# Kernel optimization log

Measured on AMD Instinct MI355X. Metric: run time of the kernel, lower is better.

## Reference

```python
import jax, jax.numpy as jnp
import numpy as np

R_EPS = 1e-15

def _sdf_net(x, W1, b1, W2, b2):
    h = jax.nn.relu(x @ W1 + b1)
    return h @ W2 + b2  # [..., 1+feat]

def _fd_gradient(x, W1, b1, W2, b2, eps):
    # central finite differences of the SDF along the 3 axes
    offs = eps * jnp.eye(3, dtype=x.dtype)              # [3,3]
    xp = x[None, :, :] + offs[:, None, :]               # [3,P,3]
    xm = x[None, :, :] - offs[:, None, :]
    sp = _sdf_net(xp, W1, b1, W2, b2)[..., 0]           # [3,P]
    sm = _sdf_net(xm, W1, b1, W2, b2)[..., 0]
    return ((sp - sm) / (2.0 * eps)).T                  # [P,3]

def _softplus100(x):
    # torch.nn.Softplus(beta=100)
    return jax.nn.softplus(100.0 * x) / 100.0

def _exclusive_cumprod(a):
    ones = jnp.ones_like(a[:, :1])
    return jnp.cumprod(jnp.concatenate([ones, a], -1), -1)[:, :-1]

def _sample_pdf(bins, weights, n_samples):
    # bins [R,K], weights [R,K-1]; deterministic inverse-CDF sampling (det=True)
    weights = weights + 1e-5
    pdf = weights / jnp.sum(weights, -1, keepdims=True)
    cdf = jnp.cumsum(pdf, -1)
    cdf = jnp.concatenate([jnp.zeros_like(cdf[:, :1]), cdf], -1)  # [R,K]
    K = cdf.shape[-1]
    u = jnp.linspace(0.5 / n_samples, 1.0 - 0.5 / n_samples, n_samples, dtype=bins.dtype)
    u = jnp.broadcast_to(u[None], (bins.shape[0], n_samples))
    inds = jax.vmap(lambda c, uu: jnp.searchsorted(c, uu, side='right'))(cdf, u)
    below = jnp.clip(inds - 1, 0, K - 1)
    above = jnp.clip(inds, 0, K - 1)
    cdf_b = jnp.take_along_axis(cdf, below, -1)
    cdf_a = jnp.take_along_axis(cdf, above, -1)
    bin_b = jnp.take_along_axis(bins, below, -1)
    bin_a = jnp.take_along_axis(bins, above, -1)
    denom = cdf_a - cdf_b
    denom = jnp.where(denom < 1e-5, jnp.ones_like(denom), denom)
    t = (u - cdf_b) / denom
    return bin_b + t * (bin_a - bin_b)

def _forward(rays_o, rays_d, W1, b1, W2, b2, Wc1, bc1, Wc2, bc2, inv_s_param,
             num_steps, upsample_steps, bound):
    B, N = rays_o.shape[:2]
    ro = rays_o.reshape(-1, 3)
    rd = rays_d.reshape(-1, 3)
    R = ro.shape[0]
    bnd = float(bound)
    # near/far from cube bound
    tmin = (-bnd - ro) / (rd + R_EPS)
    tmax = (bnd - ro) / (rd + R_EPS)
    near = jnp.max(jnp.minimum(tmin, tmax), -1, keepdims=True)
    far = jnp.min(jnp.maximum(tmin, tmax), -1, keepdims=True)
    near = jnp.maximum(near, 0.05)
    z = jnp.linspace(0.0, 1.0, num_steps, dtype=ro.dtype)[None]
    z_vals = near + (far - near) * z                     # [R,S0]
    sample_dist = (far - near) / num_steps               # [R,1]
    pts = ro[:, None, :] + rd[:, None, :] * z_vals[..., None]
    pts = jnp.clip(pts, -bnd, bnd)
    # --- coarse SDF pass + inverse-CDF importance resampling (torch.no_grad) ---
    sdf_c = _sdf_net(pts.reshape(-1, 3), W1, b1, W2, b2)[:, 0].reshape(R, num_steps)
    sdf_c = jax.lax.stop_gradient(sdf_c)
    d_c = z_vals[:, 1:] - z_vals[:, :-1]
    mid_sdf = 0.5 * (sdf_c[:, 1:] + sdf_c[:, :-1])
    cos_val = jnp.clip((sdf_c[:, 1:] - sdf_c[:, :-1]) / (d_c + 1e-5), -1e3, 0.0)
    prev_c = jax.nn.sigmoid((mid_sdf - cos_val * d_c * 0.5) * 64.0)
    next_c = jax.nn.sigmoid((mid_sdf + cos_val * d_c * 0.5) * 64.0)
    alpha_c = jnp.clip((prev_c - next_c + 1e-5) / (prev_c + 1e-5), 0.0, 1.0)
    w_c = alpha_c * _exclusive_cumprod(1.0 - alpha_c + 1e-7)
    new_z = jax.lax.stop_gradient(_sample_pdf(z_vals, w_c, upsample_steps))
    z_vals = jnp.sort(jnp.concatenate([z_vals, new_z], -1), -1)
    S = num_steps + upsample_steps
    # --- fine pass: deltas / midpoints / shading / NeuS compositing ---
    deltas = z_vals[:, 1:] - z_vals[:, :-1]
    deltas = jnp.concatenate([deltas, jnp.broadcast_to(sample_dist, (R, 1))], -1)
    z_mid = jnp.concatenate([z_vals[:, :-1] + 0.5 * deltas[:, :-1], z_vals[:, -1:]], -1)
    new_pts = ro[:, None, :] + rd[:, None, :] * z_mid[..., None]
    new_pts = jnp.clip(new_pts, -bnd, bnd)
    flat_pts = new_pts.reshape(-1, 3)                    # [R*S,3]
    out = _sdf_net(flat_pts, W1, b1, W2, b2)
    sdf = out[:, :1]
    feat = out[:, 1:]
    grad = _fd_gradient(flat_pts, W1, b1, W2, b2, 0.005)  # eps=0.005*(1-ratio), ratio=0
    normal = grad / (1e-5 + jnp.linalg.norm(grad, axis=-1, keepdims=True))
    dirs = jnp.broadcast_to(rd[:, None, :], new_pts.shape).reshape(-1, 3)
    cin = jnp.concatenate([flat_pts, dirs, normal, feat], -1)
    color = jax.nn.sigmoid(jax.nn.relu(cin @ Wc1 + bc1) @ Wc2 + bc2)   # [R*S,3]
    inv_s = jnp.exp(10.0 * inv_s_param)                   # forward_variance()
    true_cos = jnp.sum(dirs * normal, -1, keepdims=True)
    iter_cos = -_softplus100(-true_cos)                   # cos_anneal_ratio = 1.0
    d_flat = deltas.reshape(-1, 1)
    prev_cdf = jax.nn.sigmoid((sdf - iter_cos * d_flat * 0.5) * inv_s)
    next_cdf = jax.nn.sigmoid((sdf + iter_cos * d_flat * 0.5) * inv_s)
    alpha = jnp.clip((prev_cdf - next_cdf + 1e-5) / (prev_cdf + 1e-5), 0.0, 1.0).reshape(R, S)
    weights = alpha * _exclusive_cumprod(1.0 - alpha + 1e-7)
    weights_sum = jnp.sum(weights, -1, keepdims=True)
    image = jnp.sum(color.reshape(R, S, 3) * weights[..., None], 1)
    image = image + (1.0 - weights_sum) * 1.0             # bg_color = 1
    return image.reshape(B, N, 3)

def setup_inputs() -> dict:
    key = jax.random.key(0)
    ks = jax.random.split(key, 8)
    B, N, H, F = 1, 4096, 64, 64
    rays_o = (jax.random.uniform(ks[0], (B, N, 3), jnp.float32) - 0.5) * 0.5
    d = jax.random.normal(ks[1], (B, N, 3), jnp.float32)
    rays_d = d / (1e-8 + jnp.linalg.norm(d, axis=-1, keepdims=True))
    def lin(k, i, o):
        return jax.random.normal(k, (i, o), jnp.float32) / np.sqrt(i).astype(np.float32)
    W1 = lin(ks[2], 3, H); b1 = jnp.zeros((H,), jnp.float32)
    W2 = lin(ks[3], H, 1 + F); b2 = jnp.zeros((1 + F,), jnp.float32)
    Wc1 = lin(ks[4], 9 + F, H); bc1 = jnp.zeros((H,), jnp.float32)
    Wc2 = lin(ks[5], H, 3); bc2 = jnp.zeros((3,), jnp.float32)
    inv_s_param = jnp.full((1,), 0.3, jnp.float32)
    return {"rays_o": rays_o, "rays_d": rays_d, "W1": W1, "b1": b1, "W2": W2, "b2": b2,
            "Wc1": Wc1, "bc1": bc1, "Wc2": Wc2, "bc2": bc2, "inv_s_param": inv_s_param,
            "num_steps": 64, "upsample_steps": 64, "bound": 1}

def reference(rays_o, rays_d, W1, b1, W2, b2, Wc1, bc1, Wc2, bc2, inv_s_param,
              num_steps, upsample_steps, bound):
    return _forward(rays_o, rays_d, W1, b1, W2, b2, Wc1, bc1, Wc2, bc2, inv_s_param,
                    num_steps, upsample_steps, bound)
```

## Files before the change

### kernel.cpp

```cpp
#include <hip/hip_runtime.h>
#include <hip/hip_bf16.h>
#include <cmath>

#define RAYS_PER_BLOCK 2
#define KS 84

#define OFF_W1    0
#define OFF_W1E   256
#define OFF_WC2   512
#define OFF_BC2   768
#define OFF_AF    772

typedef __attribute__((ext_vector_type(4))) short  short4v;
typedef __attribute__((ext_vector_type(8))) short  short8v;
typedef __attribute__((ext_vector_type(16))) float f32x16;

__device__ __forceinline__ float sigm(float x){ return 1.0f/(1.0f + expf(-x)); }
__device__ __forceinline__ float clampf(float x, float lo, float hi){ return fminf(fmaxf(x, lo), hi); }
__device__ __forceinline__ unsigned short f2bf(float x){
  __hip_bfloat16 h = __float2bfloat16(x);
  return *reinterpret_cast<unsigned short*>(&h);
}
__device__ __forceinline__ unsigned pk2(float a, float b){
  return (unsigned)f2bf(a) | ((unsigned)f2bf(b) << 16);
}
__device__ __forceinline__ short8v lds_load8(const unsigned short* p){
  short4v lo = *(const short4v*)p;
  short4v hi = *(const short4v*)(p + 4);
  short8v r;
  r[0]=lo[0]; r[1]=lo[1]; r[2]=lo[2]; r[3]=lo[3];
  r[4]=hi[0]; r[5]=hi[1]; r[6]=hi[2]; r[7]=hi[3];
  return r;
}

__global__ void prep_weights(const float* __restrict__ W1, const float* __restrict__ b1,
                             const float* __restrict__ W2, const float* __restrict__ b2,
                             const float* __restrict__ Wc1, const float* __restrict__ bc1,
                             const float* __restrict__ Wc2, const float* __restrict__ bc2,
                             float* __restrict__ ws)
{
  int g = blockIdx.x * blockDim.x + threadIdx.x;
  if (g < 640){
    int f = g >> 6, ln = g & 63;
    int mb = f / 5, kk = f - 5*mb;
    int c  = 32*mb + (ln & 31);
    int kbase = 16*kk + 8*(ln >> 5);
    unsigned short* dst = ((unsigned short*)(ws + OFF_AF)) + (size_t)g * 8;
    for (int j = 0; j < 8; ++j){
      int k = kbase + j;
      float v;
      if (k < 64){
        v = 0.f;
        for (int t = 0; t < 64; ++t) v += W2[k*65 + 1 + t] * Wc1[(9+t)*64 + c];
      } else if (k < 73){
        v = Wc1[(k-64)*64 + c];
      } else if (k == 73){
        v = bc1[c];
        for (int t = 0; t < 64; ++t) v += b2[1+t] * Wc1[(9+t)*64 + c];
      } else v = 0.f;
      dst[j] = f2bf(v);
    }
  } else if (g < 704){
    int j = g - 640;
    ws[OFF_W1 + 4*j + 0] = W1[j];
    ws[OFF_W1 + 4*j + 1] = W1[64+j];
    ws[OFF_W1 + 4*j + 2] = W1[128+j];
    ws[OFF_W1 + 4*j + 3] = b1[j];
  } else if (g < 768){
    int j = g - 704;
    ws[OFF_W1E + 4*j + 0] = 0.005f * W1[j];
    ws[OFF_W1E + 4*j + 1] = 0.005f * W1[64+j];
    ws[OFF_W1E + 4*j + 2] = 0.005f * W1[128+j];
    ws[OFF_W1E + 4*j + 3] = W2[j*65];
  } else if (g < 832){
    int j = g - 768;
    ws[OFF_WC2 + 4*j + 0] = Wc2[j*3+0];
    ws[OFF_WC2 + 4*j + 1] = Wc2[j*3+1];
    ws[OFF_WC2 + 4*j + 2] = Wc2[j*3+2];
    ws[OFF_WC2 + 4*j + 3] = 0.f;
  } else if (g < 836){
    int j = g - 832;
    ws[OFF_BC2 + j] = (j < 3) ? bc2[j] : b2[0];
  }
}

__global__ __launch_bounds__(256)
void neus_render(const float* __restrict__ rays_o, const float* __restrict__ rays_d,
                 const float* __restrict__ inv_s_p, const float* __restrict__ ws,
                 float* __restrict__ out)
{
  __shared__ unsigned short s_aext[4][64*KS];
  __shared__ float4 s_wc2[64];
  __shared__ float  s_z[RAYS_PER_BLOCK][64];
  __shared__ float  s_cdf[RAYS_PER_BLOCK][64];
  __shared__ float  s_newz[RAYS_PER_BLOCK][64];
  __shared__ float  s_zall[RAYS_PER_BLOCK][128];
  __shared__ float  s_red[RAYS_PER_BLOCK][2][4];
  __shared__ float  s_wtot[RAYS_PER_BLOCK][2];

  const int tid  = threadIdx.x;
  const int rs   = tid >> 7;
  const int lt   = tid & 127;
  const int lane = tid & 63;
  const int wir  = (tid >> 6) & 1;
  const int wv   = tid >> 6;
  const int ray  = blockIdx.x * RAYS_PER_BLOCK + rs;

  const float4* __restrict__ pW1  = (const float4*)(ws + OFF_W1);
  const float4* __restrict__ pW1E = (const float4*)(ws + OFF_W1E);
  const float*  __restrict__ pbc2 = ws + OFF_BC2;
  const float b20 = pbc2[3];

  if (tid < 64) s_wc2[tid] = ((const float4*)(ws + OFF_WC2))[tid];

  float ox = rays_o[ray*3], oy = rays_o[ray*3+1], oz = rays_o[ray*3+2];
  float dx = rays_d[ray*3], dy = rays_d[ray*3+1], dz = rays_d[ray*3+2];
  float tnx = (-1.f-ox)/(dx+1e-15f), tfx = (1.f-ox)/(dx+1e-15f);
  float tny = (-1.f-oy)/(dy+1e-15f), tfy = (1.f-oy)/(dy+1e-15f);
  float tnz = (-1.f-oz)/(dz+1e-15f), tfz = (1.f-oz)/(dz+1e-15f);
  float nearv = fmaxf(fmaxf(fminf(tnx,tfx), fminf(tny,tfy)), fminf(tnz,tfz));
  float farv  = fminf(fminf(fmaxf(tnx,tfx), fmaxf(tny,tfy)), fmaxf(tnz,tfz));
  nearv = fmaxf(nearv, 0.05f);
  const float sd = (farv - nearv) * (1.f/64.f);

  if (wir == 0){
    float zt = nearv + (farv-nearv) * ((float)lane * (1.f/63.f));
    float px = clampf(ox + dx*zt, -1.f, 1.f);
    float py = clampf(oy + dy*zt, -1.f, 1.f);
    float pz = clampf(oz + dz*zt, -1.f, 1.f);
    float acc = b20;
    #pragma unroll 8
    for (int j = 0; j < 64; ++j){
      float4 w = pW1[j];
      acc += fmaxf(px*w.x + py*w.y + pz*w.z + w.w, 0.f) * ws[OFF_W1E + 4*j + 3];
    }
    s_z[rs][lane] = zt;
    float s1  = __shfl_down(acc, 1);
    float zt1 = nearv + (farv-nearv) * ((float)(lane+1) * (1.f/63.f));
    float a_c = 0.f, qv = 1.f;
    if (lane < 63){
      float dc   = zt1 - zt;
      float mid  = 0.5f*(acc + s1);
      float cosv = clampf((s1-acc)/(dc+1e-5f), -1000.f, 0.f);
      float est  = cosv*dc*0.5f;
      float pcv  = sigm((mid-est)*64.f);
      float ncv  = sigm((mid+est)*64.f);
      a_c = clampf((pcv-ncv+1e-5f)/(pcv+1e-5f), 0.f, 1.f);
      qv  = 1.f - a_c + 1e-7f;
    }
    float p = qv;
    #pragma unroll
    for (int off = 1; off < 64; off <<= 1){
      float t = __shfl_up(p, off);
      if (lane >= off) p *= t;
    }
    float ec = __shfl_up(p, 1);
    if (lane == 0) ec = 1.f;
    float wvv = (lane < 63) ? (a_c*ec + 1e-5f) : 0.f;
    float tot = wvv;
    #pragma unroll
    for (int off = 32; off > 0; off >>= 1) tot += __shfl_xor(tot, off);
    float cs = wvv;
    #pragma unroll
    for (int off = 1; off < 64; off <<= 1){
      float t = __shfl_up(cs, off);
      if (lane >= off) cs += t;
    }
    if (lane == 0)  s_cdf[rs][0] = 0.f;
    if (lane < 63)  s_cdf[rs][lane+1] = cs / tot;
  }
  __syncthreads();

  if (wir == 0){
    float u = ((float)lane + 0.5f) * (1.f/64.f);
    int lo = 0, hi = 64;
    while (lo < hi){
      int m = (lo+hi) >> 1;
      if (s_cdf[rs][m] <= u) lo = m+1; else hi = m;
    }
    int below = lo - 1;
    int above = lo < 63 ? lo : 63;
    float cb = s_cdf[rs][below], ca = s_cdf[rs][above];
    float bb = s_z[rs][below],   ba = s_z[rs][above];
    float den = ca - cb; if (den < 1e-5f) den = 1.f;
    float tt = (u - cb)/den;
    s_newz[rs][lane] = bb + tt*(ba - bb);
  }
  __syncthreads();

  {
    float v; int pos;
    if (lt < 64){
      v = s_z[rs][lt];
      int lo = 0, hi = 64;
      while (lo < hi){ int m=(lo+hi)>>1; if (s_newz[rs][m] < v) lo = m+1; else hi = m; }
      pos = lt + lo;
    } else {
      int jj = lt - 64;
      v = s_newz[rs][jj];
      int lo = 0, hi = 64;
      while (lo < hi){ int m=(lo+hi)>>1; if (s_z[rs][m] <= v) lo = m+1; else hi = m; }
      pos = jj + lo;
    }
    s_zall[rs][pos] = v;
  }
  __syncthreads();

  float zc = s_zall[rs][lt];
  float zn = s_zall[rs][lt < 127 ? lt+1 : 127];
  float delta = (lt < 127) ? (zn - zc) : sd;
  float zm    = (lt < 127) ? (zc + 0.5f*delta) : zc;
  float px = clampf(ox + dx*zm, -1.f, 1.f);
  float py = clampf(oy + dy*zm, -1.f, 1.f);
  float pz = clampf(oz + dz*zm, -1.f, 1.f);

  unsigned short* arow = &s_aext[wv][(unsigned)lane * KS];
  float sa = b20;
  float a0=b20,a1=b20,a2=b20,a3=b20,a4=b20,a5=b20;
  #pragma unroll 2
  for (int j2 = 0; j2 < 32; ++j2){
    int j = 2*j2;
    float4 w0 = pW1[j],   e0 = pW1E[j];
    float4 w1 = pW1[j+1], e1 = pW1E[j+1];
    float base0 = fmaf(px, w0.x, fmaf(py, w0.y, fmaf(pz, w0.z, w0.w)));
    float base1 = fmaf(px, w1.x, fmaf(py, w1.y, fmaf(pz, w1.z, w1.w)));
    float hv0 = fmaxf(base0, 0.f), hv1 = fmaxf(base1, 0.f);
    sa = fmaf(hv0, e0.w, sa); sa = fmaf(hv1, e1.w, sa);
    a0 = fmaf(fmaxf(base0+e0.x,0.f), e0.w, a0); a0 = fmaf(fmaxf(base1+e1.x,0.f), e1.w, a0);
    a1 = fmaf(fmaxf(base0-e0.x,0.f), e0.w, a1); a1 = fmaf(fmaxf(base1-e1.x,0.f), e1.w, a1);
    a2 = fmaf(fmaxf(base0+e0.y,0.f), e0.w, a2); a2 = fmaf(fmaxf(base1+e1.y,0.f), e1.w, a2);
    a3 = fmaf(fmaxf(base0-e0.y,0.f), e0.w, a3); a3 = fmaf(fmaxf(base1-e1.y,0.f), e1.w, a3);
    a4 = fmaf(fmaxf(base0+e0.z,0.f), e0.w, a4); a4 = fmaf(fmaxf(base1+e1.z,0.f), e1.w, a4);
    a5 = fmaf(fmaxf(base0-e0.z,0.f), e0.w, a5); a5 = fmaf(fmaxf(base1-e1.z,0.f), e1.w, a5);
    *(unsigned*)&arow[j] = pk2(hv0, hv1);
  }
  float sdfv = sa;
  float gx = (a0-a1)*100.f, gy = (a2-a3)*100.f, gz = (a4-a5)*100.f;
  float gn = 1e-5f + sqrtf(gx*gx + gy*gy + gz*gz);
  float nx = gx/gn, ny = gy/gn, nz = gz/gn;

  *(unsigned*)&arow[64] = pk2(px, py);
  *(unsigned*)&arow[66] = pk2(pz, dx);
  *(unsigned*)&arow[68] = pk2(dy, dz);
  *(unsigned*)&arow[70] = pk2(nx, ny);
  *(unsigned*)&arow[72] = pk2(nz, 1.0f);
  *(unsigned*)&arow[74] = 0u;
  *(unsigned*)&arow[76] = 0u;
  *(unsigned*)&arow[78] = 0u;

  const short8v* pAF = (const short8v*)(ws + OFF_AF);
  short8v af[10];
  #pragma unroll
  for (int f = 0; f < 10; ++f) af[f] = pAF[f*64 + lane];

  __builtin_amdgcn_wave_barrier();

  f32x16 acc00, acc01, acc10, acc11;
  #pragma unroll
  for (int i = 0; i < 16; ++i){ acc00[i]=0.f; acc01[i]=0.f; acc10[i]=0.f; acc11[i]=0.f; }
  const unsigned short* aw = s_aext[wv];
  const int scol = lane & 31;
  const int half8 = (lane >> 5) * 8;
  #pragma unroll
  for (int kk = 0; kk < 5; ++kk){
    int koff = 16*kk + half8;
    short8v b0 = lds_load8(&aw[ scol      * KS + koff]);
    short8v b1 = lds_load8(&aw[(32+scol) * KS + koff]);
    acc00 = __builtin_amdgcn_mfma_f32_32x32x16_bf16(af[kk],   b0, acc00, 0, 0, 0);
    acc10 = __builtin_amdgcn_mfma_f32_32x32x16_bf16(af[5+kk], b0, acc10, 0, 0, 0);
    acc01 = __builtin_amdgcn_mfma_f32_32x32x16_bf16(af[kk],   b1, acc01, 0, 0, 0);
    acc11 = __builtin_amdgcn_mfma_f32_32x32x16_bf16(af[5+kk], b1, acc11, 0, 0, 0);
  }

  float pr0=0.f,pr1=0.f,pr2=0.f,pr3=0.f,pr4=0.f,pr5=0.f;
  const int halfoff = (lane >> 5) * 4;
  #pragma unroll
  for (int r = 0; r < 16; ++r){
    int ci = (r & 3) + 8*(r >> 2) + halfoff;
    float4 wA = s_wc2[ci];
    float4 wB = s_wc2[32 + ci];
    float v;
    v = fmaxf(acc00[r], 0.f); pr0 = fmaf(v, wA.x, pr0); pr1 = fmaf(v, wA.y, pr1); pr2 = fmaf(v, wA.z, pr2);
    v = fmaxf(acc10[r], 0.f); pr0 = fmaf(v, wB.x, pr0); pr1 = fmaf(v, wB.y, pr1); pr2 = fmaf(v, wB.z, pr2);
    v = fmaxf(acc01[r], 0.f); pr3 = fmaf(v, wA.x, pr3); pr4 = fmaf(v, wA.y, pr4); pr5 = fmaf(v, wA.z, pr5);
    v = fmaxf(acc11[r], 0.f); pr3 = fmaf(v, wB.x, pr3); pr4 = fmaf(v, wB.y, pr4); pr5 = fmaf(v, wB.z, pr5);
  }
  pr0 += __shfl_xor(pr0, 32); pr1 += __shfl_xor(pr1, 32); pr2 += __shfl_xor(pr2, 32);
  pr3 += __shfl_xor(pr3, 32); pr4 += __shfl_xor(pr4, 32); pr5 += __shfl_xor(pr5, 32);
  const bool hihalf = (lane >= 32);
  float c0 = sigm((hihalf ? pr3 : pr0) + pbc2[0]);
  float c1 = sigm((hihalf ? pr4 : pr1) + pbc2[1]);
  float c2 = sigm((hihalf ? pr5 : pr2) + pbc2[2]);

  const float inv_s = expf(10.f * inv_s_p[0]);
  float tcos = dx*nx + dy*ny + dz*nz;
  float aarg = -100.f * tcos;
  float spv  = (aarg > 0.f) ? (aarg + log1pf(expf(-aarg))) : log1pf(expf(aarg));
  float iter_cos = -(spv * 0.01f);
  float est = iter_cos * delta * 0.5f;
  float pcv = sigm((sdfv - est)*inv_s);
  float ncv = sigm((sdfv + est)*inv_s);
  float alpha = clampf((pcv - ncv + 1e-5f)/(pcv + 1e-5f), 0.f, 1.f);

  float qv = 1.f - alpha + 1e-7f;
  float p = qv;
  #pragma unroll
  for (int off = 1; off < 64; off <<= 1){
    float t = __shfl_up(p, off);
    if (lane >= off) p *= t;
  }
  if (lane == 63) s_wtot[rs][wir] = p;
  __syncthreads();
  float excl = __shfl_up(p, 1);
  if (lane == 0) excl = 1.f;
  if (wir == 1) excl *= s_wtot[rs][0];
  float w  = alpha * excl;
  float r0 = w, r1 = w*c0, r2 = w*c1, r3 = w*c2;
  #pragma unroll
  for (int off = 32; off > 0; off >>= 1){
    r0 += __shfl_xor(r0, off);
    r1 += __shfl_xor(r1, off);
    r2 += __shfl_xor(r2, off);
    r3 += __shfl_xor(r3, off);
  }
  if (lane == 0){
    s_red[rs][wir][0]=r0; s_red[rs][wir][1]=r1; s_red[rs][wir][2]=r2; s_red[rs][wir][3]=r3;
  }
  __syncthreads();
  if (lt == 0){
    float wsum = s_red[rs][0][0] + s_red[rs][1][0];
    float bg = 1.f - wsum;
    out[ray*3+0] = s_red[rs][0][1] + s_red[rs][1][1] + bg;
    out[ray*3+1] = s_red[rs][0][2] + s_red[rs][1][2] + bg;
    out[ray*3+2] = s_red[rs][0][3] + s_red[rs][1][3] + bg;
  }
}

extern "C" void kernel_launch(void* const* d_in, const int* in_sizes, int n_in,
                              void* d_out, int out_size, void* d_ws, size_t ws_size,
                              hipStream_t stream)
{
  const float* rays_o = (const float*)d_in[0];
  const float* rays_d = (const float*)d_in[1];
  const float* W1  = (const float*)d_in[2];
  const float* b1  = (const float*)d_in[3];
  const float* W2  = (const float*)d_in[4];
  const float* b2  = (const float*)d_in[5];
  const float* Wc1 = (const float*)d_in[6];
  const float* bc1 = (const float*)d_in[7];
  const float* Wc2 = (const float*)d_in[8];
  const float* bc2 = (const float*)d_in[9];
  const float* inv_s = (const float*)d_in[10];
  float* out = (float*)d_out;
  float* ws  = (float*)d_ws;

  prep_weights<<<4, 256, 0, stream>>>(W1, b1, W2, b2, Wc1, bc1, Wc2, bc2, ws);

  const int R = in_sizes[0] / 3;
  dim3 grid(R / RAYS_PER_BLOCK), block(256);
  neus_render<<<grid, block, 0, stream>>>(rays_o, rays_d, inv_s, ws, out);
}
```

Baseline: 145.8 us.

## Fold weight preprocessing into render kernel, computing fused W2·Wc1 per block via MFMA

Removes the separate prep_weights launch. Each render block now builds the fused colour-layer weight matrix in shared memory: it stages W2 transposed as bf16 and multiplies it with Wc1 using MFMA, then loads the A fragments from LDS. W1, W1E and Wc2 are also staged into LDS instead of being read from the workspace. This saves a kernel launch and a serial dependency, but every one of the 2048 blocks repeats the weight GEMM and extra global loads, and adds two block-wide barriers before any ray work starts.

Result: slower. 151.1 us (+3.6%).

```diff
diff --git a/kernel.cpp b/kernel.cpp
--- a/kernel.cpp
+++ b/kernel.cpp
@@ -4,12 +4,6 @@
 
 #define RAYS_PER_BLOCK 2
 #define KS 84
-
-#define OFF_W1    0
-#define OFF_W1E   256
-#define OFF_WC2   512
-#define OFF_BC2   768
-#define OFF_AF    772
 
 typedef __attribute__((ext_vector_type(4))) short  short4v;
 typedef __attribute__((ext_vector_type(8))) short  short8v;
@@ -33,63 +27,17 @@
   return r;
 }
 
-__global__ void prep_weights(const float* __restrict__ W1, const float* __restrict__ b1,
-                             const float* __restrict__ W2, const float* __restrict__ b2,
-                             const float* __restrict__ Wc1, const float* __restrict__ bc1,
-                             const float* __restrict__ Wc2, const float* __restrict__ bc2,
-                             float* __restrict__ ws)
-{
-  int g = blockIdx.x * blockDim.x + threadIdx.x;
-  if (g < 640){
-    int f = g >> 6, ln = g & 63;
-    int mb = f / 5, kk = f - 5*mb;
-    int c  = 32*mb + (ln & 31);
-    int kbase = 16*kk + 8*(ln >> 5);
-    unsigned short* dst = ((unsigned short*)(ws + OFF_AF)) + (size_t)g * 8;
-    for (int j = 0; j < 8; ++j){
-      int k = kbase + j;
-      float v;
-      if (k < 64){
-        v = 0.f;
-        for (int t = 0; t < 64; ++t) v += W2[k*65 + 1 + t] * Wc1[(9+t)*64 + c];
-      } else if (k < 73){
-        v = Wc1[(k-64)*64 + c];
-      } else if (k == 73){
-        v = bc1[c];
-        for (int t = 0; t < 64; ++t) v += b2[1+t] * Wc1[(9+t)*64 + c];
-      } else v = 0.f;
-      dst[j] = f2bf(v);
-    }
-  } else if (g < 704){
-    int j = g - 640;
-    ws[OFF_W1 + 4*j + 0] = W1[j];
-    ws[OFF_W1 + 4*j + 1] = W1[64+j];
-    ws[OFF_W1 + 4*j + 2] = W1[128+j];
-    ws[OFF_W1 + 4*j + 3] = b1[j];
-  } else if (g < 768){
-    int j = g - 704;
-    ws[OFF_W1E + 4*j + 0] = 0.005f * W1[j];
-    ws[OFF_W1E + 4*j + 1] = 0.005f * W1[64+j];
-    ws[OFF_W1E + 4*j + 2] = 0.005f * W1[128+j];
-    ws[OFF_W1E + 4*j + 3] = W2[j*65];
-  } else if (g < 832){
-    int j = g - 768;
-    ws[OFF_WC2 + 4*j + 0] = Wc2[j*3+0];
-    ws[OFF_WC2 + 4*j + 1] = Wc2[j*3+1];
-    ws[OFF_WC2 + 4*j + 2] = Wc2[j*3+2];
-    ws[OFF_WC2 + 4*j + 3] = 0.f;
-  } else if (g < 836){
-    int j = g - 832;
-    ws[OFF_BC2 + j] = (j < 3) ? bc2[j] : b2[0];
-  }
-}
-
 __global__ __launch_bounds__(256)
 void neus_render(const float* __restrict__ rays_o, const float* __restrict__ rays_d,
-                 const float* __restrict__ inv_s_p, const float* __restrict__ ws,
-                 float* __restrict__ out)
+                 const float* __restrict__ W1, const float* __restrict__ b1,
+                 const float* __restrict__ W2, const float* __restrict__ b2,
+                 const float* __restrict__ Wc1, const float* __restrict__ bc1,
+                 const float* __restrict__ Wc2, const float* __restrict__ bc2,
+                 const float* __restrict__ inv_s_p, float* __restrict__ out)
 {
-  __shared__ unsigned short s_aext[4][64*KS];
+  __shared__ unsigned short SU[4*64*KS];
+  __shared__ float4 s_w1[64];
+  __shared__ float4 s_w1e[64];
   __shared__ float4 s_wc2[64];
   __shared__ float  s_z[RAYS_PER_BLOCK][64];
   __shared__ float  s_cdf[RAYS_PER_BLOCK][64];
@@ -98,20 +46,76 @@
   __shared__ float  s_red[RAYS_PER_BLOCK][2][4];
   __shared__ float  s_wtot[RAYS_PER_BLOCK][2];
 
+  unsigned short* ABUF = SU;
+  unsigned short* W2T  = SU + 64*KS;
+
   const int tid  = threadIdx.x;
   const int rs   = tid >> 7;
   const int lt   = tid & 127;
   const int lane = tid & 63;
   const int wir  = (tid >> 6) & 1;
   const int wv   = tid >> 6;
+  const int l31  = lane & 31;
+  const int h    = lane >> 5;
   const int ray  = blockIdx.x * RAYS_PER_BLOCK + rs;
 
-  const float4* __restrict__ pW1  = (const float4*)(ws + OFF_W1);
-  const float4* __restrict__ pW1E = (const float4*)(ws + OFF_W1E);
-  const float*  __restrict__ pbc2 = ws + OFF_BC2;
-  const float b20 = pbc2[3];
-
-  if (tid < 64) s_wc2[tid] = ((const float4*)(ws + OFF_WC2))[tid];
+  const float b20 = b2[0];
+
+  for (int i = tid; i < 4096; i += 256){
+    int k = i >> 6, t = i & 63;
+    W2T[k*KS + t] = f2bf(W2[k*65 + 1 + t]);
+  }
+  if (tid < 64){
+    int j = tid;
+    s_w1[j]  = make_float4(W1[j], W1[64+j], W1[128+j], b1[j]);
+    s_w1e[j] = make_float4(0.005f*W1[j], 0.005f*W1[64+j], 0.005f*W1[128+j], W2[j*65]);
+    s_wc2[j] = make_float4(Wc2[j*3], Wc2[j*3+1], Wc2[j*3+2], 0.f);
+  }
+  for (int i = tid; i < 576; i += 256){
+    int ii = i >> 6, c = i & 63;
+    ABUF[c*KS + 64 + ii] = f2bf(Wc1[ii*64 + c]);
+  }
+  for (int i = tid; i < 384; i += 256){
+    int z = i >> 6, c = i & 63;
+    ABUF[c*KS + 74 + z] = 0;
+  }
+  if (wv == 3){
+    float acc = bc1[lane];
+    #pragma unroll 4
+    for (int t = 0; t < 64; ++t) acc = fmaf(b2[1+t], Wc1[(9+t)*64 + lane], acc);
+    ABUF[lane*KS + 73] = f2bf(acc);
+  }
+  __syncthreads();
+
+  {
+    const int mb = wv & 1, kb = wv >> 1;
+    f32x16 e;
+    #pragma unroll
+    for (int i = 0; i < 16; ++i) e[i] = 0.f;
+    #pragma unroll
+    for (int s = 0; s < 4; ++s){
+      short8v afr;
+      #pragma unroll
+      for (int j = 0; j < 8; ++j)
+        afr[j] = (short)f2bf(Wc1[(9 + 16*s + 8*h + j)*64 + 32*mb + l31]);
+      short8v bfr = lds_load8(&W2T[(32*kb + l31)*KS + 16*s + 8*h]);
+      e = __builtin_amdgcn_mfma_f32_32x32x16_bf16(afr, bfr, e, 0, 0, 0);
+    }
+    const int kcol = 32*kb + l31;
+    #pragma unroll
+    for (int r = 0; r < 16; ++r){
+      int c = 32*mb + (r & 3) + 8*(r >> 2) + 4*h;
+      ABUF[c*KS + kcol] = f2bf(e[r]);
+    }
+  }
+  __syncthreads();
+
+  short8v af[10];
+  #pragma unroll
+  for (int f = 0; f < 10; ++f){
+    int mb = f / 5, kk = f - 5*mb;
+    af[f] = lds_load8(&ABUF[(32*mb + l31)*KS + 16*kk + 8*h]);
+  }
 
   float ox = rays_o[ray*3], oy = rays_o[ray*3+1], oz = rays_o[ray*3+2];
   float dx = rays_d[ray*3], dy = rays_d[ray*3+1], dz = rays_d[ray*3+2];
@@ -131,8 +135,8 @@
     float acc = b20;
     #pragma unroll 8
     for (int j = 0; j < 64; ++j){
-      float4 w = pW1[j];
-      acc += fmaxf(px*w.x + py*w.y + pz*w.z + w.w, 0.f) * ws[OFF_W1E + 4*j + 3];
+      float4 w = s_w1[j];
+      acc += fmaxf(px*w.x + py*w.y + pz*w.z + w.w, 0.f) * s_w1e[j].w;
     }
     s_z[rs][lane] = zt;
     float s1  = __shfl_down(acc, 1);
@@ -214,14 +218,14 @@
   float py = clampf(oy + dy*zm, -1.f, 1.f);
   float pz = clampf(oz + dz*zm, -1.f, 1.f);
 
-  unsigned short* arow = &s_aext[wv][(unsigned)lane * KS];
+  unsigned short* arow = &SU[wv*64*KS + (unsigned)lane * KS];
   float sa = b20;
   float a0=b20,a1=b20,a2=b20,a3=b20,a4=b20,a5=b20;
   #pragma unroll 2
   for (int j2 = 0; j2 < 32; ++j2){
     int j = 2*j2;
-    float4 w0 = pW1[j],   e0 = pW1E[j];
-    float4 w1 = pW1[j+1], e1 = pW1E[j+1];
+    float4 w0 = s_w1[j],   e0 = s_w1e[j];
+    float4 w1 = s_w1[j+1], e1 = s_w1e[j+1];
     float base0 = fmaf(px, w0.x, fmaf(py, w0.y, fmaf(pz, w0.z, w0.w)));
     float base1 = fmaf(px, w1.x, fmaf(py, w1.y, fmaf(pz, w1.z, w1.w)));
     float hv0 = fmaxf(base0, 0.f), hv1 = fmaxf(base1, 0.f);
@@ -248,22 +252,16 @@
   *(unsigned*)&arow[76] = 0u;
   *(unsigned*)&arow[78] = 0u;
 
-  const short8v* pAF = (const short8v*)(ws + OFF_AF);
-  short8v af[10];
-  #pragma unroll
-  for (int f = 0; f < 10; ++f) af[f] = pAF[f*64 + lane];
-
   __builtin_amdgcn_wave_barrier();
 
   f32x16 acc00, acc01, acc10, acc11;
   #pragma unroll
   for (int i = 0; i < 16; ++i){ acc00[i]=0.f; acc01[i]=0.f; acc10[i]=0.f; acc11[i]=0.f; }
-  const unsigned short* aw = s_aext[wv];
-  const int scol = lane & 31;
-  const int half8 = (lane >> 5) * 8;
+  const unsigned short* aw = &SU[wv*64*KS];
+  const int scol = l31;
   #pragma unroll
   for (int kk = 0; kk < 5; ++kk){
-    int koff = 16*kk + half8;
+    int koff = 16*kk + 8*h;
     short8v b0 = lds_load8(&aw[ scol      * KS + koff]);
     short8v b1 = lds_load8(&aw[(32+scol) * KS + koff]);
     acc00 = __builtin_amdgcn_mfma_f32_32x32x16_bf16(af[kk],   b0, acc00, 0, 0, 0);
@@ -273,7 +271,7 @@
   }
 
   float pr0=0.f,pr1=0.f,pr2=0.f,pr3=0.f,pr4=0.f,pr5=0.f;
-  const int halfoff = (lane >> 5) * 4;
+  const int halfoff = h * 4;
   #pragma unroll
   for (int r = 0; r < 16; ++r){
     int ci = (r & 3) + 8*(r >> 2) + halfoff;
@@ -288,9 +286,9 @@
   pr0 += __shfl_xor(pr0, 32); pr1 += __shfl_xor(pr1, 32); pr2 += __shfl_xor(pr2, 32);
   pr3 += __shfl_xor(pr3, 32); pr4 += __shfl_xor(pr4, 32); pr5 += __shfl_xor(pr5, 32);
   const bool hihalf = (lane >= 32);
-  float c0 = sigm((hihalf ? pr3 : pr0) + pbc2[0]);
-  float c1 = sigm((hihalf ? pr4 : pr1) + pbc2[1]);
-  float c2 = sigm((hihalf ? pr5 : pr2) + pbc2[2]);
+  float c0 = sigm((hihalf ? pr3 : pr0) + bc2[0]);
+  float c1 = sigm((hihalf ? pr4 : pr1) + bc2[1]);
+  float c2 = sigm((hihalf ? pr5 : pr2) + bc2[2]);
 
   const float inv_s = expf(10.f * inv_s_p[0]);
   float tcos = dx*nx + dy*ny + dz*nz;
@@ -352,11 +350,9 @@
   const float* bc2 = (const float*)d_in[9];
   const float* inv_s = (const float*)d_in[10];
   float* out = (float*)d_out;
-  float* ws  = (float*)d_ws;
-
-  prep_weights<<<4, 256, 0, stream>>>(W1, b1, W2, b2, Wc1, bc1, Wc2, bc2, ws);
 
   const int R = in_sizes[0] / 3;
   dim3 grid(R / RAYS_PER_BLOCK), block(256);
-  neus_render<<<grid, block, 0, stream>>>(rays_o, rays_d, inv_s, ws, out);
-}
+  neus_render<<<grid, block, 0, stream>>>(rays_o, rays_d, W1, b1, W2, b2,
+                                          Wc1, bc1, Wc2, bc2, inv_s, out);
+}
```
